# Kernel optimization log

Measured on AMD Instinct MI355X. Metric: run time of the kernel, lower is better.

The kernel has to match this reference:

```python
import jax, jax.numpy as jnp
import numpy as np


def setup_inputs() -> dict:
    key = jax.random.key(0)
    kE, kD, kW, kU, kV = jax.random.split(key, 5)
    B, T, H, U = 32, 2048, 1024, 1024
    scale = 0.02
    return {
        "enc_out": jax.random.normal(kE, (B, T, H), dtype=jnp.float32),
        "dec_hidden": jax.random.normal(kD, (B, H), dtype=jnp.float32),
        "Wa": jax.random.normal(kW, (H, U), dtype=jnp.float32) * scale,
        "Ua": jax.random.normal(kU, (H, U), dtype=jnp.float32) * scale,
        "Va": jax.random.normal(kV, (U,), dtype=jnp.float32) * scale,
    }


def reference(enc_out, dec_hidden, Wa, Ua, Va):
    # Bahdanau additive attention.
    # enc_out: [B, T, H]; dec_hidden: [B, H]; Wa: [H, U]; Ua: [H, U]; Va: [U]
    dec_proj = jnp.einsum("bh,hu->bu", dec_hidden, Wa)          # [B, U]
    enc_proj = jnp.einsum("bth,hu->btu", enc_out, Ua)            # [B, T, U]
    s = jnp.tanh(enc_proj + dec_proj[:, None, :])                # [B, T, U]
    score = jnp.einsum("btu,u->bt", s, Va)                       # [B, T]
    alpha = jax.nn.softmax(score, axis=-1)                       # [B, T]
    context = jnp.einsum("bt,bth->bh", alpha, enc_out)           # [B, H]
    return context
```

## Files before the change

### kernel.cpp

```cpp
#include <hip/hip_runtime.h>
#include <stdint.h>


#define B_ 32
#define T_ 2048
#define H_ 1024
#define U_ 1024
#define M_ (B_ * T_)

typedef __bf16 bf16x8 __attribute__((ext_vector_type(8)));
typedef float f32x4 __attribute__((ext_vector_type(4)));

__device__ __forceinline__ unsigned f2b(float f) {
  unsigned u = __float_as_uint(f);
  return (u + 0x7FFFu + ((u >> 16) & 1u)) >> 16;
}
__device__ __forceinline__ float b2f(unsigned short u) {
  return __uint_as_float(((unsigned)u) << 16);
}
__device__ __forceinline__ float fast_tanh(float x) {
  float xc = fminf(fmaxf(x, -12.f), 12.f);
  float t = exp2f(xc * 2.885390081777927f);
  return (t - 1.f) * __builtin_amdgcn_rcpf(t + 1.f);
}

#define AS1 __attribute__((address_space(1)))
#define AS3 __attribute__((address_space(3)))
__device__ __forceinline__ void gld_lds16(const void* g, void* l) {
  __builtin_amdgcn_global_load_lds((AS1 const void*)g, (AS3 void*)l, 16, 0, 0);
}

__global__ __launch_bounds__(256) void prep_k(
    const float4* __restrict__ enc, uint4* __restrict__ outA,
    const float* __restrict__ Ua, uint4* __restrict__ Ub,
    const float* __restrict__ dh, const float* __restrict__ Wa,
    float* __restrict__ dp4, float* __restrict__ outz) {
  const int bx = blockIdx.x;
  const int tx = threadIdx.x;

  if (bx < 4096) {
    __shared__ uint4 L4[128 * 17];
    const int band = bx;
    const int mt = band >> 3;
    const int R = (band & 7) << 4;
    const float4* src = enc + (size_t)band * 4096;
#pragma unroll
    for (int i = 0; i < 8; ++i) {
      int p = i * 256 + tx;
      int r = p >> 7, pc = p & 127;
      float4 a = src[r * 256 + pc * 2];
      float4 b = src[r * 256 + pc * 2 + 1];
      uint4 o;
      o.x = f2b(a.x) | (f2b(a.y) << 16);
      o.y = f2b(a.z) | (f2b(a.w) << 16);
      o.z = f2b(b.x) | (f2b(b.y) << 16);
      o.w = f2b(b.z) | (f2b(b.w) << 16);
      L4[pc * 17 + r] = o;
    }
    __syncthreads();
    const int r2 = tx & 15, kq = (tx >> 4) & 3, w = tx >> 6;
#pragma unroll
    for (int j = 0; j < 8; ++j) {
      int k8 = j * 16 + w * 4 + kq;
      outA[((size_t)mt * 128 + k8) * 128 + R + r2] = L4[k8 * 17 + r2];
    }
  } else if (bx < 4608) {
    int id = (bx - 4096) * 256 + tx;
    int h8 = id >> 10, u = id & 1023;
    const float* p = Ua + (size_t)(h8 << 3) * U_ + u;
    uint4 o;
    o.x = f2b(p[0]) | (f2b(p[U_]) << 16);
    o.y = f2b(p[2 * U_]) | (f2b(p[3 * U_]) << 16);
    o.z = f2b(p[4 * U_]) | (f2b(p[5 * U_]) << 16);
    o.w = f2b(p[6 * U_]) | (f2b(p[7 * U_]) << 16);
    Ub[(size_t)h8 * U_ + u] = o;
  } else if (bx < 5120) {
    int g = bx - 4608;
    const int u = (g & 3) * 256 + tx;
    const int b = (g >> 2) & 31, hz = g >> 7;
    const float* d = dh + b * H_ + hz * 256;
    const float* w = Wa + (size_t)(hz * 256) * U_ + u;
    float a0 = 0.f, a1 = 0.f, a2 = 0.f, a3 = 0.f;
#pragma unroll 4
    for (int h = 0; h < 256; h += 4) {
      a0 = fmaf(d[h + 0], w[(size_t)(h + 0) * U_], a0);
      a1 = fmaf(d[h + 1], w[(size_t)(h + 1) * U_], a1);
      a2 = fmaf(d[h + 2], w[(size_t)(h + 2) * U_], a2);
      a3 = fmaf(d[h + 3], w[(size_t)(h + 3) * U_], a3);
    }
    dp4[((hz * B_ + b) * U_) + u] = (a0 + a1) + (a2 + a3);
  } else {
    outz[(bx - 5120) * 256 + tx] = 0.f;
  }
}

__global__ __launch_bounds__(256, 2) void score_gemm_k(
    const unsigned short* __restrict__ encA,
    const unsigned short* __restrict__ Ub,
    const float* __restrict__ dp4,
    const float* __restrict__ Va,
    float* __restrict__ score8)
{
  __shared__ union {
    struct {
      alignas(16) unsigned short As[8][128][8];
      alignas(16) unsigned short Bs[8][128][8];
    } t;
    float sred[128 * 33];
  } sm;

  const int bx = blockIdx.x;
  const int mtile = ((bx >> 6) << 3) | (bx & 7), ntile = (bx >> 3) & 7;
  const int m0 = mtile << 7, n0 = ntile << 7;
  const int tid = threadIdx.x;
  const int wv = tid >> 6, ln = tid & 63;
  const int wm = wv & 1, wn = wv >> 1;
  const int quad = ln >> 4, l16 = ln & 15;

  f32x4 acc[4][4];
  const f32x4 zero = {0.f, 0.f, 0.f, 0.f};
#pragma unroll
  for (int i = 0; i < 4; ++i)
#pragma unroll
    for (int j = 0; j < 4; ++j) acc[i][j] = zero;

  const unsigned short* encT = encA + (size_t)mtile * (128 * 128 * 8);

  for (int k0 = 0; k0 < H_; k0 += 64) {
    __syncthreads();
#pragma unroll
    for (int c = 0; c < 4; ++c) {
      int chunk = (wv << 2) + c;
      int k8 = chunk >> 1, half = chunk & 1;
      const unsigned short* ga =
          encT + (((size_t)((k0 >> 3) + k8) * 128) + (half << 6) + ln) * 8;
      gld_lds16(ga, &sm.t.As[k8][half << 6][0]);
      const unsigned short* gb =
          Ub + (((size_t)((k0 >> 3) + k8) * U_) + n0 + (half << 6) + ln) * 8;
      gld_lds16(gb, &sm.t.Bs[k8][half << 6][0]);
    }
    __syncthreads();

#pragma unroll
    for (int kk = 0; kk < 2; ++kk) {
      int k8b = (kk << 2) + quad;
      bf16x8 af[4], bf[4];
#pragma unroll
      for (int mt = 0; mt < 4; ++mt)
        af[mt] = *(const bf16x8*)&sm.t.As[k8b][(wm << 6) + (mt << 4) + l16][0];
#pragma unroll
      for (int nt = 0; nt < 4; ++nt)
        bf[nt] = *(const bf16x8*)&sm.t.Bs[k8b][(wn << 6) + (nt << 4) + l16][0];
#pragma unroll
      for (int mt = 0; mt < 4; ++mt)
#pragma unroll
        for (int nt = 0; nt < 4; ++nt)
          acc[mt][nt] = __builtin_amdgcn_mfma_f32_16x16x32_bf16(
              af[mt], bf[nt], acc[mt][nt], 0, 0, 0);
    }
  }

  const int bq = m0 >> 11;
  float va[4], dpv[4];
#pragma unroll
  for (int nt = 0; nt < 4; ++nt) {
    int col = n0 + (wn << 6) + (nt << 4) + l16;
    va[nt] = Va[col];
    dpv[nt] = dp4[bq * U_ + col] + dp4[B_ * U_ + bq * U_ + col] +
              dp4[2 * B_ * U_ + bq * U_ + col] + dp4[3 * B_ * U_ + bq * U_ + col];
  }
  __syncthreads();
#pragma unroll
  for (int mt = 0; mt < 4; ++mt) {
#pragma unroll
    for (int r = 0; r < 4; ++r) {
      float v = 0.f;
#pragma unroll
      for (int nt = 0; nt < 4; ++nt)
        v += fast_tanh(acc[mt][nt][r] + dpv[nt]) * va[nt];
      int row = (wm << 6) + (mt << 4) + (quad << 2) + r;
      sm.sred[row * 33 + (wn << 4) + l16] = v;
    }
  }
  __syncthreads();
  if (tid < 128) {
    const float* p = &sm.sred[tid * 33];
    float s = 0.f;
#pragma unroll
    for (int j = 0; j < 32; ++j) s += p[j];
    score8[(size_t)ntile * M_ + m0 + tid] = s;
  }
}

__global__ __launch_bounds__(256) void ctx_k(const uint4* __restrict__ encA,
                                             const float* __restrict__ score8,
                                             float* __restrict__ out) {
  const int b = blockIdx.y, bt = blockIdx.x, tid = threadIdx.x;
  __shared__ float s_sc[2048];
  __shared__ float a_s[128];
  __shared__ float red[4];
  __shared__ float cred[2][128][8];

  float4 v0 = {0.f, 0.f, 0.f, 0.f}, v1 = {0.f, 0.f, 0.f, 0.f};
#pragma unroll
  for (int k = 0; k < 8; ++k) {
    const float4* p = (const float4*)(score8 + (size_t)k * M_ + b * T_);
    float4 x0 = p[tid * 2], x1 = p[tid * 2 + 1];
    v0.x += x0.x; v0.y += x0.y; v0.z += x0.z; v0.w += x0.w;
    v1.x += x1.x; v1.y += x1.y; v1.z += x1.z; v1.w += x1.w;
  }
  ((float4*)s_sc)[tid * 2] = v0;
  ((float4*)s_sc)[tid * 2 + 1] = v1;

  float m = fmaxf(fmaxf(fmaxf(v0.x, v0.y), fmaxf(v0.z, v0.w)),
                  fmaxf(fmaxf(v1.x, v1.y), fmaxf(v1.z, v1.w)));
#pragma unroll
  for (int off = 32; off >= 1; off >>= 1) m = fmaxf(m, __shfl_xor(m, off));
  if ((tid & 63) == 0) red[tid >> 6] = m;
  __syncthreads();
  m = fmaxf(fmaxf(red[0], red[1]), fmaxf(red[2], red[3]));
  __syncthreads();

  const float l2e = 1.4426950408889634f;
  float sum = exp2f((v0.x - m) * l2e) + exp2f((v0.y - m) * l2e) +
              exp2f((v0.z - m) * l2e) + exp2f((v0.w - m) * l2e) +
              exp2f((v1.x - m) * l2e) + exp2f((v1.y - m) * l2e) +
              exp2f((v1.z - m) * l2e) + exp2f((v1.w - m) * l2e);
#pragma unroll
  for (int off = 32; off >= 1; off >>= 1) sum += __shfl_xor(sum, off);
  if ((tid & 63) == 0) red[tid >> 6] = sum;
  __syncthreads();
  const float inv = 1.f / (red[0] + red[1] + red[2] + red[3]);

  if (tid < 128) a_s[tid] = exp2f((s_sc[bt * 128 + tid] - m) * l2e) * inv;
  __syncthreads();

  const int tx = tid & 127, th = tid >> 7;
  const int mt = b * 16 + bt;
  const uint4* base = encA + ((size_t)mt * 128 + tx) * 128 + th * 64;
  float a[8];
#pragma unroll
  for (int j = 0; j < 8; ++j) a[j] = 0.f;
#pragma unroll 4
  for (int i = 0; i < 64; ++i) {
    float w = a_s[th * 64 + i];
    uint4 e = base[i];
    a[0] = fmaf(w, b2f((unsigned short)e.x), a[0]);
    a[1] = fmaf(w, b2f((unsigned short)(e.x >> 16)), a[1]);
    a[2] = fmaf(w, b2f((unsigned short)e.y), a[2]);
    a[3] = fmaf(w, b2f((unsigned short)(e.y >> 16)), a[3]);
    a[4] = fmaf(w, b2f((unsigned short)e.z), a[4]);
    a[5] = fmaf(w, b2f((unsigned short)(e.z >> 16)), a[5]);
    a[6] = fmaf(w, b2f((unsigned short)e.w), a[6]);
    a[7] = fmaf(w, b2f((unsigned short)(e.w >> 16)), a[7]);
  }
#pragma unroll
  for (int j = 0; j < 8; ++j) cred[th][tx][j] = a[j];
  __syncthreads();
  if (th == 0) {
    float* o = out + (size_t)b * H_ + tx * 8;
#pragma unroll
    for (int j = 0; j < 8; ++j)
      atomicAdd(&o[j], cred[0][tx][j] + cred[1][tx][j]);
  }
}

extern "C" void kernel_launch(void* const* d_in, const int* in_sizes, int n_in,
                              void* d_out, int out_size, void* d_ws, size_t ws_size,
                              hipStream_t stream) {
  const float* enc = (const float*)d_in[0];
  const float* dh  = (const float*)d_in[1];
  const float* Wa  = (const float*)d_in[2];
  const float* Ua  = (const float*)d_in[3];
  const float* Va  = (const float*)d_in[4];

  char* ws = (char*)d_ws;
  unsigned short* encA = (unsigned short*)ws;
  unsigned short* Ub   = (unsigned short*)(ws + 134217728);
  float* dp4    = (float*)(ws + 136314880);
  float* score8 = (float*)(ws + 136839168);

  prep_k<<<5248, 256, 0, stream>>>((const float4*)enc, (uint4*)encA, Ua,
                                   (uint4*)Ub, dh, Wa, dp4, (float*)d_out);
  score_gemm_k<<<4096, 256, 0, stream>>>(encA, Ub, dp4, Va, score8);
  ctx_k<<<dim3(16, 32), 256, 0, stream>>>((const uint4*)encA, score8,
                                          (float*)d_out);
}
```

Baseline: 562.1 us.

## Double-buffer LDS tiles in score GEMM to overlap global loads with MFMA

Doubles the LDS A/B tile buffers in the score GEMM and issues the next k-tile's global-to-LDS loads before computing on the current one. Explicit vmcnt waits and scheduling barriers replace the two syncthreads per iteration. The aim is to hide global load latency behind MFMA work. The cost is twice the LDS footprint (64KB), which may limit occupancy at two blocks per CU.

Measured after the change: 569.3 us. Within noise of the previous version (+1.3%).

```diff
diff --git a/kernel.cpp b/kernel.cpp
--- a/kernel.cpp
+++ b/kernel.cpp
@@ -28,6 +28,12 @@
 #define AS3 __attribute__((address_space(3)))
 __device__ __forceinline__ void gld_lds16(const void* g, void* l) {
   __builtin_amdgcn_global_load_lds((AS1 const void*)g, (AS3 void*)l, 16, 0, 0);
+}
+
+__device__ __forceinline__ void BAR() {
+  __builtin_amdgcn_sched_barrier(0);
+  __builtin_amdgcn_s_barrier();
+  __builtin_amdgcn_sched_barrier(0);
 }
 
 __global__ __launch_bounds__(256) void prep_k(
@@ -103,8 +109,8 @@
 {
   __shared__ union {
     struct {
-      alignas(16) unsigned short As[8][128][8];
-      alignas(16) unsigned short Bs[8][128][8];
+      alignas(16) unsigned short As[2][8][128][8];
+      alignas(16) unsigned short Bs[2][8][128][8];
     } t;
     float sred[128 * 33];
   } sm;
@@ -126,20 +132,32 @@
 
   const unsigned short* encT = encA + (size_t)mtile * (128 * 128 * 8);
 
-  for (int k0 = 0; k0 < H_; k0 += 64) {
-    __syncthreads();
+  auto STAGE = [&](int kt, int bsel) {
+    const int kb = kt << 3;
 #pragma unroll
     for (int c = 0; c < 4; ++c) {
       int chunk = (wv << 2) + c;
-      int k8 = chunk >> 1, half = chunk & 1;
+      int k8 = chunk >> 1, half = (chunk & 1) << 6;
       const unsigned short* ga =
-          encT + (((size_t)((k0 >> 3) + k8) * 128) + (half << 6) + ln) * 8;
-      gld_lds16(ga, &sm.t.As[k8][half << 6][0]);
+          encT + (((size_t)(kb + k8) * 128) + half + ln) * 8;
+      gld_lds16(ga, &sm.t.As[bsel][k8][half][0]);
       const unsigned short* gb =
-          Ub + (((size_t)((k0 >> 3) + k8) * U_) + n0 + (half << 6) + ln) * 8;
-      gld_lds16(gb, &sm.t.Bs[k8][half << 6][0]);
-    }
-    __syncthreads();
+          Ub + (((size_t)(kb + k8) * U_) + n0 + half + ln) * 8;
+      gld_lds16(gb, &sm.t.Bs[bsel][k8][half][0]);
+    }
+  };
+
+  STAGE(0, 0);
+
+  for (int kt = 0; kt < 16; ++kt) {
+    const int cb = kt & 1, nb = cb ^ 1;
+    if (kt < 15) {
+      STAGE(kt + 1, nb);
+      asm volatile("s_waitcnt vmcnt(8)" ::: "memory");
+    } else {
+      asm volatile("s_waitcnt vmcnt(0)" ::: "memory");
+    }
+    BAR();
 
 #pragma unroll
     for (int kk = 0; kk < 2; ++kk) {
@@ -147,10 +165,12 @@
       bf16x8 af[4], bf[4];
 #pragma unroll
       for (int mt = 0; mt < 4; ++mt)
-        af[mt] = *(const bf16x8*)&sm.t.As[k8b][(wm << 6) + (mt << 4) + l16][0];
+        af[mt] =
+            *(const bf16x8*)&sm.t.As[cb][k8b][(wm << 6) + (mt << 4) + l16][0];
 #pragma unroll
       for (int nt = 0; nt < 4; ++nt)
-        bf[nt] = *(const bf16x8*)&sm.t.Bs[k8b][(wn << 6) + (nt << 4) + l16][0];
+        bf[nt] =
+            *(const bf16x8*)&sm.t.Bs[cb][k8b][(wn << 6) + (nt << 4) + l16][0];
 #pragma unroll
       for (int mt = 0; mt < 4; ++mt)
 #pragma unroll
@@ -158,6 +178,7 @@
           acc[mt][nt] = __builtin_amdgcn_mfma_f32_16x16x32_bf16(
               af[mt], bf[nt], acc[mt][nt], 0, 0, 0);
     }
+    BAR();
   }
 
   const int bq = m0 >> 11;
```

## Switch score GEMM to 32x32x16 MFMA with shuffle-based epilogue reduction

Applied to the files above, without the earlier changes.

Replaces the 16x16x32 bf16 MFMA tiling (4x4 tiles per wave) with 32x32x16 MFMA (2x2 tiles per wave). This halves the LDS fragment loads per k-step and uses the larger MFMA shape. The epilogue now reduces tanh*Va across lanes with xor shuffles instead of a padded shared-memory row sum, which shrinks LDS use. Launch bounds are raised to request 4 blocks per CU, which may force register spilling given the 64 accumulator floats per thread. The shuffle reduction adds 5 shuffle steps for each of 32 rows.

Result: slower. 586.7 us (+4.4%).

```diff
diff --git a/kernel.cpp b/kernel.cpp
--- a/kernel.cpp
+++ b/kernel.cpp
@@ -9,7 +9,7 @@
 #define M_ (B_ * T_)
 
 typedef __bf16 bf16x8 __attribute__((ext_vector_type(8)));
-typedef float f32x4 __attribute__((ext_vector_type(4)));
+typedef float f32x16 __attribute__((ext_vector_type(16)));
 
 __device__ __forceinline__ unsigned f2b(float f) {
   unsigned u = __float_as_uint(f);
@@ -94,7 +94,7 @@
   }
 }
 
-__global__ __launch_bounds__(256, 2) void score_gemm_k(
+__global__ __launch_bounds__(256, 4) void score_gemm_k(
     const unsigned short* __restrict__ encA,
     const unsigned short* __restrict__ Ub,
     const float* __restrict__ dp4,
@@ -106,7 +106,7 @@
       alignas(16) unsigned short As[8][128][8];
       alignas(16) unsigned short Bs[8][128][8];
     } t;
-    float sred[128 * 33];
+    float sred[128][2];
   } sm;
 
   const int bx = blockIdx.x;
@@ -115,14 +115,15 @@
   const int tid = threadIdx.x;
   const int wv = tid >> 6, ln = tid & 63;
   const int wm = wv & 1, wn = wv >> 1;
-  const int quad = ln >> 4, l16 = ln & 15;
-
-  f32x4 acc[4][4];
-  const f32x4 zero = {0.f, 0.f, 0.f, 0.f};
-#pragma unroll
-  for (int i = 0; i < 4; ++i)
-#pragma unroll
-    for (int j = 0; j < 4; ++j) acc[i][j] = zero;
+  const int l32 = ln & 31, lh = ln >> 5;
+
+  f32x16 acc[2][2];
+#pragma unroll
+  for (int i = 0; i < 2; ++i)
+#pragma unroll
+    for (int j = 0; j < 2; ++j)
+#pragma unroll
+      for (int r = 0; r < 16; ++r) acc[i][j][r] = 0.f;
 
   const unsigned short* encT = encA + (size_t)mtile * (128 * 128 * 8);
 
@@ -142,53 +143,52 @@
     __syncthreads();
 
 #pragma unroll
-    for (int kk = 0; kk < 2; ++kk) {
-      int k8b = (kk << 2) + quad;
-      bf16x8 af[4], bf[4];
-#pragma unroll
-      for (int mt = 0; mt < 4; ++mt)
-        af[mt] = *(const bf16x8*)&sm.t.As[k8b][(wm << 6) + (mt << 4) + l16][0];
-#pragma unroll
-      for (int nt = 0; nt < 4; ++nt)
-        bf[nt] = *(const bf16x8*)&sm.t.Bs[k8b][(wn << 6) + (nt << 4) + l16][0];
-#pragma unroll
-      for (int mt = 0; mt < 4; ++mt)
-#pragma unroll
-        for (int nt = 0; nt < 4; ++nt)
-          acc[mt][nt] = __builtin_amdgcn_mfma_f32_16x16x32_bf16(
-              af[mt], bf[nt], acc[mt][nt], 0, 0, 0);
+    for (int kk = 0; kk < 4; ++kk) {
+      const int k8b = (kk << 1) + lh;
+      bf16x8 af[2], bf[2];
+#pragma unroll
+      for (int mi = 0; mi < 2; ++mi)
+        af[mi] = *(const bf16x8*)&sm.t.As[k8b][(wm << 6) + (mi << 5) + l32][0];
+#pragma unroll
+      for (int ni = 0; ni < 2; ++ni)
+        bf[ni] = *(const bf16x8*)&sm.t.Bs[k8b][(wn << 6) + (ni << 5) + l32][0];
+#pragma unroll
+      for (int mi = 0; mi < 2; ++mi)
+#pragma unroll
+        for (int ni = 0; ni < 2; ++ni)
+          acc[mi][ni] = __builtin_amdgcn_mfma_f32_32x32x16_bf16(
+              af[mi], bf[ni], acc[mi][ni], 0, 0, 0);
     }
   }
 
   const int bq = m0 >> 11;
-  float va[4], dpv[4];
-#pragma unroll
-  for (int nt = 0; nt < 4; ++nt) {
-    int col = n0 + (wn << 6) + (nt << 4) + l16;
-    va[nt] = Va[col];
-    dpv[nt] = dp4[bq * U_ + col] + dp4[B_ * U_ + bq * U_ + col] +
-              dp4[2 * B_ * U_ + bq * U_ + col] + dp4[3 * B_ * U_ + bq * U_ + col];
-  }
-  __syncthreads();
-#pragma unroll
-  for (int mt = 0; mt < 4; ++mt) {
-#pragma unroll
-    for (int r = 0; r < 4; ++r) {
-      float v = 0.f;
-#pragma unroll
-      for (int nt = 0; nt < 4; ++nt)
-        v += fast_tanh(acc[mt][nt][r] + dpv[nt]) * va[nt];
-      int row = (wm << 6) + (mt << 4) + (quad << 2) + r;
-      sm.sred[row * 33 + (wn << 4) + l16] = v;
+  float va[2], dpv[2];
+#pragma unroll
+  for (int ni = 0; ni < 2; ++ni) {
+    int col = n0 + (wn << 6) + (ni << 5) + l32;
+    va[ni] = Va[col];
+    dpv[ni] = dp4[bq * U_ + col] + dp4[B_ * U_ + bq * U_ + col] +
+              dp4[2 * B_ * U_ + bq * U_ + col] +
+              dp4[3 * B_ * U_ + bq * U_ + col];
+  }
+  __syncthreads();
+#pragma unroll
+  for (int mi = 0; mi < 2; ++mi) {
+#pragma unroll
+    for (int r = 0; r < 16; ++r) {
+      float v = fast_tanh(acc[mi][0][r] + dpv[0]) * va[0] +
+                fast_tanh(acc[mi][1][r] + dpv[1]) * va[1];
+#pragma unroll
+      for (int off = 1; off < 32; off <<= 1) v += __shfl_xor(v, off);
+      if (l32 == 0) {
+        int row = (wm << 6) + (mi << 5) + (r & 3) + ((r >> 2) << 3) + (lh << 2);
+        sm.sred[row][wn] = v;
+      }
     }
   }
   __syncthreads();
   if (tid < 128) {
-    const float* p = &sm.sred[tid * 33];
-    float s = 0.f;
-#pragma unroll
-    for (int j = 0; j < 32; ++j) s += p[j];
-    score8[(size_t)ntile * M_ + m0 + tid] = s;
+    score8[(size_t)ntile * M_ + m0 + tid] = sm.sred[tid][0] + sm.sred[tid][1];
   }
 }
 
```
